# Kernel tuning notes

Hardware: AMD Instinct MI355X
Metric: run time of the kernel (lower is better)

Reference implementation:

```python
import jax, jax.numpy as jnp
import numpy as np

N, E = 100000, 1600000
F_IN, HID, C, L = 512, 128, 64, 64
ALPHA, THETA = 0.1, 0.5


def setup_inputs() -> dict:
    key = jax.random.key(0)
    ks = jax.random.split(key, 6)
    x = jax.random.normal(ks[0], (N, F_IN), jnp.float32)
    edge_index = jax.random.randint(ks[1], (2, E), 0, N, jnp.int32)
    W_in = jax.random.normal(ks[2], (F_IN, HID), jnp.float32) * (1.0 / np.sqrt(F_IN))
    b_in = jnp.zeros((HID,), jnp.float32)
    W_convs = jax.random.normal(ks[3], (L, HID, HID), jnp.float32) * (1.0 / np.sqrt(HID))
    W_out = jax.random.normal(ks[4], (HID, C), jnp.float32) * (1.0 / np.sqrt(HID))
    b_out = jnp.zeros((C,), jnp.float32)
    return {"x": x, "edge_index": edge_index, "W_in": W_in, "b_in": b_in,
            "W_convs": W_convs, "W_out": W_out, "b_out": b_out}


def reference(x, edge_index, W_in, b_in, W_convs, W_out, b_out):
    src, dst = edge_index[0], edge_index[1]
    # gcn_norm with self loops: A_hat = D^-1/2 (A + I) D^-1/2
    deg = jax.ops.segment_sum(jnp.ones((E,), x.dtype), dst, num_segments=N) + 1.0
    dinv = jax.lax.rsqrt(deg)
    ew = dinv[src] * dinv[dst]          # [E] off-diagonal weights
    self_w = dinv * dinv                # [N] self-loop weights

    def spmm(h):  # h: [N, HID]
        agg = jax.ops.segment_sum(h[src] * ew[:, None], dst, num_segments=N)
        return agg + self_w[:, None] * h

    # beta_l = log(theta / l + 1), l = 1..L
    betas = jnp.log(THETA / jnp.arange(1, L + 1, dtype=x.dtype) + 1.0)

    x0 = jax.nn.relu(x @ W_in + b_in)   # [N, HID]

    def layer(h, lw):
        W, beta = lw
        p = spmm(h)
        t = (1.0 - ALPHA) * p + ALPHA * x0          # initial residual
        out = (1.0 - beta) * t + beta * (t @ W)     # identity mapping (shared weights)
        return jax.nn.relu(out), None

    z, _ = jax.lax.scan(layer, x0, (W_convs, betas))
    logits = z @ W_out + b_out
    return z, jax.nn.log_softmax(logits, axis=-1)
```

## Files before the change

### kernel.cpp

```cpp
#include <hip/hip_runtime.h>
#include <hip/hip_bf16.h>

#define NN 100000
#define NE 1600000
#define F_IN 512
#define HID 128
#define C_OUT 64
#define L_LAYERS 64
#define SCAN_NB 98

using short8 = __attribute__((ext_vector_type(8))) short;
using f32x4  = __attribute__((ext_vector_type(4))) float;
typedef __attribute__((ext_vector_type(4))) unsigned short ushort4v;

__device__ __forceinline__ short f2bf(float f) {
    __hip_bfloat16 h = __float2bfloat16(f);
    return __builtin_bit_cast(short, h);
}
__device__ __forceinline__ unsigned short f2bfu(float f) {
    __hip_bfloat16 h = __float2bfloat16(f);
    return __builtin_bit_cast(unsigned short, h);
}
__device__ __forceinline__ float bflo(unsigned u) { return __uint_as_float(u << 16); }
__device__ __forceinline__ float bfhi(unsigned u) { return __uint_as_float(u & 0xffff0000u); }
__device__ __forceinline__ float bf2f(unsigned short u) { return __uint_as_float((unsigned)u << 16); }


__global__ void count_deg(const int* __restrict__ dst, int* __restrict__ cnt) {
    int e = blockIdx.x * blockDim.x + threadIdx.x;
    if (e < NE) atomicAdd(&cnt[dst[e]], 1);
}

__global__ void compute_dinv(const int* __restrict__ cnt, float* __restrict__ dinv) {
    int n = blockIdx.x * blockDim.x + threadIdx.x;
    if (n < NN) dinv[n] = rsqrtf((float)cnt[n] + 1.0f);
}

__global__ __launch_bounds__(256) void scan1(const int* __restrict__ cnt,
                                             int* __restrict__ row_ptr,
                                             int* __restrict__ partial) {
    __shared__ int sdata[256];
    int tid = threadIdx.x;
    int base = blockIdx.x * 1024;
    int v[4];
    int idx0 = base + tid * 4;
#pragma unroll
    for (int i = 0; i < 4; ++i) {
        int idx = idx0 + i;
        v[i] = (idx < NN) ? cnt[idx] : 0;
    }
    int s = v[0] + v[1] + v[2] + v[3];
    sdata[tid] = s;
    __syncthreads();
    int x = s;
    for (int off = 1; off < 256; off <<= 1) {
        int y = (tid >= off) ? sdata[tid - off] : 0;
        __syncthreads();
        x += y;
        sdata[tid] = x;
        __syncthreads();
    }
    int run = x - s;
#pragma unroll
    for (int i = 0; i < 4; ++i) {
        int idx = idx0 + i;
        if (idx < NN) row_ptr[idx] = run;
        run += v[i];
    }
    if (tid == 255) partial[blockIdx.x] = x;
}

__global__ __launch_bounds__(128) void scan2(int* __restrict__ partial) {
    __shared__ int sdata[128];
    int tid = threadIdx.x;
    int v = (tid < SCAN_NB) ? partial[tid] : 0;
    sdata[tid] = v;
    __syncthreads();
    int x = v;
    for (int off = 1; off < 128; off <<= 1) {
        int y = (tid >= off) ? sdata[tid - off] : 0;
        __syncthreads();
        x += y;
        sdata[tid] = x;
        __syncthreads();
    }
    if (tid < SCAN_NB) partial[tid] = x - v;
}

__global__ void scan3(int* __restrict__ row_ptr, const int* __restrict__ partial) {
    int idx = blockIdx.x * blockDim.x + threadIdx.x;
    if (idx < NN) row_ptr[idx] += partial[idx >> 10];
    else if (idx <= NN + 64) row_ptr[idx] = NE;
}

__global__ void scatter_csr(const int* __restrict__ src, const int* __restrict__ dst,
                            const float* __restrict__ dinv, int* __restrict__ fill,
                            int2* __restrict__ edges) {
    int e = blockIdx.x * blockDim.x + threadIdx.x;
    if (e >= NE) return;
    int s = src[e], d = dst[e];
    int pos = atomicAdd(&fill[d], 1);
    edges[pos] = make_int2(s, __float_as_int(dinv[s] * dinv[d]));
}

__global__ __launch_bounds__(256) void prep_wt(const float* __restrict__ Wc,
                                               const float* __restrict__ Win,
                                               __hip_bfloat16* __restrict__ WT,
                                               __hip_bfloat16* __restrict__ WinT) {
    int b = blockIdx.x, tid = threadIdx.x;
    if (b < 64) {
        const float* src = Wc + (size_t)b * HID * HID;
        __hip_bfloat16* dstp = WT + (size_t)b * HID * HID;
        for (int it = 0; it < 64; ++it) {
            int idx = it * 256 + tid;
            int n = idx >> 7, k = idx & 127;
            dstp[idx] = __float2bfloat16(src[k * HID + n]);
        }
    } else {
        int j = b - 64;
        for (int it = 0; it < 16; ++it) {
            int gid = j * 4096 + it * 256 + tid;
            int n = gid >> 9, k = gid & 511;
            WinT[gid] = __float2bfloat16(Win[k * HID + n]);
        }
    }
}

#define LOAD_SET(X0V, X1V, WVV, KT)                                              \
    {                                                                            \
        int k0_ = (KT) * 32;                                                     \
        _Pragma("unroll")                                                        \
        for (int i = 0; i < 2; ++i) {                                            \
            int id = i * 256 + tid;                                              \
            int rr = id >> 2, slot = id & 3;                                     \
            int grow = row0 + rr;                                                \
            X0V[i] = make_float4(0.f, 0.f, 0.f, 0.f); X1V[i] = X0V[i];           \
            if (grow < NN) {                                                     \
                X0V[i] = *(const float4*)&X[(size_t)grow * F_IN + k0_ + slot * 8];     \
                X1V[i] = *(const float4*)&X[(size_t)grow * F_IN + k0_ + slot * 8 + 4]; \
            }                                                                    \
            WVV[i] = *(const uint4*)&WinT[(size_t)rr * F_IN + k0_ + slot * 8];   \
        }                                                                        \
    }

#define PHASE(X0V, X1V, WVV, KT, BUF)                                            \
    {                                                                            \
        short* Xs = SMEM + (BUF) * 4096;                                         \
        short* Wsh = SMEM + 8192 + (BUF) * 4096;                                 \
        _Pragma("unroll")                                                        \
        for (int i = 0; i < 2; ++i) {                                            \
            int id = i * 256 + tid;                                              \
            int rr = id >> 2, slot = id & 3;                                     \
            short8 p;                                                            \
            p[0] = f2bf(X0V[i].x); p[1] = f2bf(X0V[i].y);                        \
            p[2] = f2bf(X0V[i].z); p[3] = f2bf(X0V[i].w);                        \
            p[4] = f2bf(X1V[i].x); p[5] = f2bf(X1V[i].y);                        \
            p[6] = f2bf(X1V[i].z); p[7] = f2bf(X1V[i].w);                        \
            *(short8*)&Xs[rr * 32 + (slot ^ ((rr >> 1) & 3)) * 8] = p;           \
            *(uint4*)&Wsh[rr * 32 + (slot ^ ((rr >> 1) & 3)) * 8] = WVV[i];      \
        }                                                                        \
        __syncthreads();                                                         \
        if ((KT) < 14) LOAD_SET(X0V, X1V, WVV, (KT) + 2);                        \
        short8 a[2], bb[8];                                                      \
        _Pragma("unroll")                                                        \
        for (int m = 0; m < 2; ++m) {                                            \
            int row = w * 32 + m * 16 + r;                                       \
            a[m] = *(short8*)&Xs[row * 32 + (g ^ ((row >> 1) & 3)) * 8];         \
        }                                                                        \
        _Pragma("unroll")                                                        \
        for (int n = 0; n < 8; ++n) {                                            \
            int row = n * 16 + r;                                                \
            bb[n] = *(short8*)&Wsh[row * 32 + (g ^ ((row >> 1) & 3)) * 8];       \
        }                                                                        \
        _Pragma("unroll")                                                        \
        for (int m = 0; m < 2; ++m)                                              \
            _Pragma("unroll")                                                    \
            for (int n = 0; n < 8; ++n)                                          \
                acc[m][n] = __builtin_amdgcn_mfma_f32_16x16x32_bf16(a[m], bb[n], acc[m][n], 0, 0, 0); \
    }

__global__ __launch_bounds__(256) void gemm_x0_mfma(const float* __restrict__ X,
                                                    const __hip_bfloat16* __restrict__ WinT,
                                                    const float* __restrict__ bias,
                                                    __hip_bfloat16* __restrict__ X0b) {
    __shared__ short SMEM[128 * 128];
    int tid = threadIdx.x;
    int w = tid >> 6, l = tid & 63, g = l >> 4, r = l & 15;
    int row0 = blockIdx.x * 128;
    f32x4 acc[2][8] = {};

    float4 ax0[2], ax1[2]; uint4 aw[2];
    float4 bx0[2], bx1[2]; uint4 bw[2];

    LOAD_SET(ax0, ax1, aw, 0);
    LOAD_SET(bx0, bx1, bw, 1);
    for (int kt = 0; kt < 16; kt += 2) {
        PHASE(ax0, ax1, aw, kt, 0);
        PHASE(bx0, bx1, bw, kt + 1, 1);
    }
    __syncthreads();
#pragma unroll
    for (int m = 0; m < 2; ++m) {
#pragma unroll
        for (int n = 0; n < 8; ++n) {
            int col = n * 16 + r;
            float bv = bias[col];
#pragma unroll
            for (int q = 0; q < 4; ++q) {
                int row = w * 32 + m * 16 + g * 4 + q;
                float v = fmaxf(acc[m][n][q] + bv, 0.f);
                SMEM[row * 128 + ((col >> 3) ^ (row & 15)) * 8 + (col & 7)] = f2bf(v);
            }
        }
    }
    __syncthreads();
#pragma unroll
    for (int i = 0; i < 8; ++i) {
        int id = i * 256 + tid;
        int rr = id >> 4, c8 = id & 15;
        int grow = row0 + rr;
        if (grow < NN)
            *(uint4*)&X0b[(size_t)grow * HID + c8 * 8] =
                *(uint4*)&SMEM[rr * 128 + ((c8 ^ (rr & 15)) * 8)];
    }
}

__global__ __launch_bounds__(512, 6) void layer_fused(const unsigned* __restrict__ H2,
                                                      const unsigned* __restrict__ X02,
                                                      const float* __restrict__ dinv,
                                                      const int* __restrict__ row_ptr,
                                                      const int2* __restrict__ edges,
                                                      const __hip_bfloat16* __restrict__ WTl,
                                                      float beta,
                                                      __hip_bfloat16* __restrict__ Hout,
                                                      float* __restrict__ Zf) {
    __shared__ short Ts[64 * 128];
    __shared__ short Ws[128 * 128];
    int tid = threadIdx.x;
    int w = tid >> 6, l = tid & 63, g = l >> 4, r = l & 15;
    int row0 = blockIdx.x * 64;

#pragma unroll
    for (int i = 0; i < 4; ++i) {
        int id = i * 512 + tid;
        int rr = id >> 4, slot = id & 15;
        uint4 wv = *(const uint4*)&WTl[(size_t)id * 8];
        *(uint4*)&Ws[rr * 128 + (slot ^ (rr & 15)) * 8] = wv;
    }

    unsigned* TsU = (unsigned*)Ts;
    int nb0 = row0 + w * 8;
    int ep[9];
#pragma unroll
    for (int k = 0; k < 9; ++k) ep[k] = __builtin_amdgcn_readfirstlane(row_ptr[nb0 + k]);

#pragma unroll
    for (int j = 0; j < 4; ++j) {
        int rrA = w * 8 + 2 * j, rrB = rrA + 1;
        int nA = row0 + rrA, nB = nA + 1;
        bool vA = nA < NN, vB = nB < NN;
        unsigned hsA = vA ? H2[((unsigned)nA << 6) + l] : 0u;
        unsigned hsB = vB ? H2[((unsigned)nB << 6) + l] : 0u;
        unsigned xvA = vA ? X02[((unsigned)nA << 6) + l] : 0u;
        unsigned xvB = vB ? X02[((unsigned)nB << 6) + l] : 0u;
        float dvA = vA ? dinv[nA] : 0.f, dvB = vB ? dinv[nB] : 0.f;
        float a0A = dvA * dvA * bflo(hsA), a1A = dvA * dvA * bfhi(hsA);
        float a0B = dvB * dvB * bflo(hsB), a1B = dvB * dvB * bfhi(hsB);
        int eA = ep[2 * j], e1A = ep[2 * j + 1];
        int eB = e1A, e1B = ep[2 * j + 2];
        while (eA < e1A || eB < e1B) {
            int cA = e1A - eA; cA = cA > 12 ? 12 : (cA < 0 ? 0 : cA);
            int cB = e1B - eB; cB = cB > 12 ? 12 : (cB < 0 ? 0 : cB);
            int sA[12], sB[12];
            float wA[12], wB[12];
#pragma unroll
            for (int u = 0; u < 12; ++u) {
                int2 t = edges[eA + u];
                sA[u] = (u < cA) ? t.x : 0;
                wA[u] = (u < cA) ? __int_as_float(t.y) : 0.f;
            }
#pragma unroll
            for (int u = 0; u < 12; ++u) {
                int2 t = edges[eB + u];
                sB[u] = (u < cB) ? t.x : 0;
                wB[u] = (u < cB) ? __int_as_float(t.y) : 0.f;
            }
            unsigned hvA[12], hvB[12];
#pragma unroll
            for (int u = 0; u < 12; ++u) hvA[u] = H2[((unsigned)sA[u] << 6) + l];
#pragma unroll
            for (int u = 0; u < 12; ++u) hvB[u] = H2[((unsigned)sB[u] << 6) + l];
#pragma unroll
            for (int u = 0; u < 12; ++u) {
                a0A = fmaf(wA[u], bflo(hvA[u]), a0A);
                a1A = fmaf(wA[u], bfhi(hvA[u]), a1A);
                a0B = fmaf(wB[u], bflo(hvB[u]), a0B);
                a1B = fmaf(wB[u], bfhi(hvB[u]), a1B);
            }
            eA += cA; eB += cB;
        }
        a0A = 0.9f * a0A + 0.1f * bflo(xvA);  a1A = 0.9f * a1A + 0.1f * bfhi(xvA);
        a0B = 0.9f * a0B + 0.1f * bflo(xvB);  a1B = 0.9f * a1B + 0.1f * bfhi(xvB);
        unsigned pkA = (unsigned)f2bfu(a0A) | ((unsigned)f2bfu(a1A) << 16);
        unsigned pkB = (unsigned)f2bfu(a0B) | ((unsigned)f2bfu(a1B) << 16);
        TsU[rrA * 64 + ((l >> 2) ^ (rrA & 15)) * 4 + (l & 3)] = pkA;
        TsU[rrB * 64 + ((l >> 2) ^ (rrB & 15)) * 4 + (l & 3)] = pkB;
    }
    __syncthreads();

    int nb = w & 3, cg = w >> 2;
    f32x4 acc[4] = {};
#pragma unroll
    for (int ks = 0; ks < 4; ++ks) {
        int rrT = nb * 16 + r;
        short8 bT = *(short8*)&Ts[rrT * 128 + ((ks * 4 + g) ^ (rrT & 15)) * 8];
        short8 aW[4];
#pragma unroll
        for (int c = 0; c < 4; ++c) {
            int rrW = (cg * 4 + c) * 16 + r;
            aW[c] = *(short8*)&Ws[rrW * 128 + ((ks * 4 + g) ^ (rrW & 15)) * 8];
        }
#pragma unroll
        for (int c = 0; c < 4; ++c)
            acc[c] = __builtin_amdgcn_mfma_f32_16x16x32_bf16(aW[c], bT, acc[c], 0, 0, 0);
    }

    float omb = 1.0f - beta;
    int node = nb * 16 + r;
    int grow = row0 + node;
    if (grow < NN) {
#pragma unroll
        for (int c = 0; c < 4; ++c) {
            int c0 = (cg * 4 + c) * 16 + g * 4;
            int slotE = c0 >> 3, posE = c0 & 7;
            ushort4v tv = *(ushort4v*)&Ts[node * 128 + (slotE ^ (node & 15)) * 8 + posE];
            float o[4];
#pragma unroll
            for (int q = 0; q < 4; ++q)
                o[q] = fmaxf(omb * bf2f(tv[q]) + beta * acc[c][q], 0.f);
            if (Zf) {
                *(float4*)&Zf[(size_t)grow * HID + c0] = make_float4(o[0], o[1], o[2], o[3]);
            } else {
                ushort4v hv;
#pragma unroll
                for (int q = 0; q < 4; ++q) hv[q] = f2bfu(o[q]);
                *(ushort4v*)&Hout[(size_t)grow * HID + c0] = hv;
            }
        }
    }
}

__global__ __launch_bounds__(256) void final_kernel(const float* __restrict__ Z,
                                                    const float* __restrict__ Wout,
                                                    const float* __restrict__ bout,
                                                    float* __restrict__ lo) {
    __shared__ float Wl[128 * 64];
    __shared__ float Zl[64][128];
    int tid = threadIdx.x;
    int w = tid >> 6, c = tid & 63;
    int n0 = blockIdx.x * 64;
#pragma unroll
    for (int i = 0; i < 8; ++i) {
        int id = i * 256 + tid;
        *(float4*)&Wl[id * 4] = *(const float4*)&Wout[(size_t)id * 4];
    }
#pragma unroll
    for (int i = 0; i < 8; ++i) {
        int id = i * 256 + tid;
        int rr = id >> 5, c4 = id & 31;
        int n = n0 + rr;
        float4 v = make_float4(0.f, 0.f, 0.f, 0.f);
        if (n < NN) v = *(const float4*)&Z[(size_t)n * HID + c4 * 4];
        *(float4*)&Zl[rr][c4 * 4] = v;
    }
    __syncthreads();
    float bv = bout[c];
#pragma unroll
    for (int i = 0; i < 4; ++i) {
        int nodeb = i * 16 + w * 4;
        float l0 = 0.f, l1 = 0.f, l2 = 0.f, l3 = 0.f;
#pragma unroll 8
        for (int k = 0; k < 128; ++k) {
            float wv = Wl[k * 64 + c];
            l0 = fmaf(Zl[nodeb + 0][k], wv, l0);
            l1 = fmaf(Zl[nodeb + 1][k], wv, l1);
            l2 = fmaf(Zl[nodeb + 2][k], wv, l2);
            l3 = fmaf(Zl[nodeb + 3][k], wv, l3);
        }
        float lg[4] = {l0 + bv, l1 + bv, l2 + bv, l3 + bv};
#pragma unroll
        for (int j = 0; j < 4; ++j) {
            float logit = lg[j];
            float m = logit;
#pragma unroll
            for (int off = 32; off; off >>= 1) m = fmaxf(m, __shfl_xor(m, off));
            float ex = __expf(logit - m);
            float ssum = ex;
#pragma unroll
            for (int off = 32; off; off >>= 1) ssum += __shfl_xor(ssum, off);
            int n = n0 + nodeb + j;
            if (n < NN) lo[(size_t)n * C_OUT + c] = logit - m - logf(ssum);
        }
    }
}

extern "C" void kernel_launch(void* const* d_in, const int* in_sizes, int n_in,
                              void* d_out, int out_size, void* d_ws, size_t ws_size,
                              hipStream_t stream) {
    const float* x = (const float*)d_in[0];
    const int* ei = (const int*)d_in[1];
    const int* src = ei;
    const int* dst = ei + NE;
    const float* W_in = (const float*)d_in[2];
    const float* b_in = (const float*)d_in[3];
    const float* W_convs = (const float*)d_in[4];
    const float* W_out = (const float*)d_in[5];
    const float* b_out = (const float*)d_in[6];
    float* out = (float*)d_out;

    char* ws = (char*)d_ws;
    float* dinv = (float*)ws;              ws += (size_t)NN * 4;
    int* row_ptr = (int*)ws;               ws += (size_t)(NN + 72) * 4;
    int* fill = (int*)ws;                  ws += (size_t)NN * 4;
    int* partial = (int*)ws;               ws += (size_t)128 * 4;
    int2* edges = (int2*)ws;               ws += (size_t)(NE + 32) * 8;
    __hip_bfloat16* WT = (__hip_bfloat16*)ws;   ws += (size_t)L_LAYERS * HID * HID * 2;
    __hip_bfloat16* WinT = (__hip_bfloat16*)ws; ws += (size_t)F_IN * HID * 2;
    __hip_bfloat16* x0b = (__hip_bfloat16*)ws;  ws += (size_t)NN * HID * 2;
    __hip_bfloat16* HbA = (__hip_bfloat16*)ws;  ws += (size_t)NN * HID * 2;
    __hip_bfloat16* HbB = (__hip_bfloat16*)ws;  ws += (size_t)NN * HID * 2;

    hipMemsetAsync(fill, 0, (size_t)NN * 4, stream);
    count_deg<<<(NE + 255) / 256, 256, 0, stream>>>(dst, fill);
    compute_dinv<<<(NN + 255) / 256, 256, 0, stream>>>(fill, dinv);
    scan1<<<SCAN_NB, 256, 0, stream>>>(fill, row_ptr, partial);
    scan2<<<1, 128, 0, stream>>>(partial);
    scan3<<<(NN + 255) / 256, 256, 0, stream>>>(row_ptr, partial);
    hipMemcpyAsync(fill, row_ptr, (size_t)NN * 4, hipMemcpyDeviceToDevice, stream);
    scatter_csr<<<(NE + 255) / 256, 256, 0, stream>>>(src, dst, dinv, fill, edges);
    prep_wt<<<80, 256, 0, stream>>>(W_convs, W_in, WT, WinT);

    int gemm_blocks = (NN + 127) / 128;
    gemm_x0_mfma<<<gemm_blocks, 256, 0, stream>>>(x, WinT, b_in, x0b);

    int layer_blocks = (NN + 63) / 64;
    float* zf = out;
    for (int l = 0; l < L_LAYERS; ++l) {
        const __hip_bfloat16* h_in = (l == 0) ? x0b : ((l & 1) ? HbA : HbB);
        __hip_bfloat16* h_out = (l & 1) ? HbB : HbA;
        float beta = logf(0.5f / (float)(l + 1) + 1.0f);
        bool last = (l == L_LAYERS - 1);
        layer_fused<<<layer_blocks, 512, 0, stream>>>(
            (const unsigned*)h_in, (const unsigned*)x0b, dinv, row_ptr, edges,
            WT + (size_t)l * HID * HID, beta,
            h_out, last ? zf : (float*)nullptr);
    }

    final_kernel<<<(NN + 63) / 64, 256, 0, stream>>>(zf, W_out, b_out, out + (size_t)NN * HID);
}
```

Before: 6.349 ms.

## Split wave across two nodes with 8-byte gathers and sort CSR neighbors

The SpMM gather now has each half-wave handle one of the two destination nodes. Each lane loads 8 bytes (4 bf16 features) per neighbor, and the per-iteration batch drops from 12 to 8 edges, which halves the number of gather instructions per edge. A new per-node bitonic sort orders each CSR row by source index to improve locality of the gathers, and a pad kernel zeroes the tail edges that unrolled loads read past the end. The added preprocessing costs one extra launch over all nodes, and the two half-waves can diverge when their node degrees differ.

```diff
diff --git a/kernel.cpp b/kernel.cpp
--- a/kernel.cpp
+++ b/kernel.cpp
@@ -101,6 +101,35 @@
     int s = src[e], d = dst[e];
     int pos = atomicAdd(&fill[d], 1);
     edges[pos] = make_int2(s, __float_as_int(dinv[s] * dinv[d]));
+}
+
+__global__ void pad_edges(int2* __restrict__ edges) {
+    int i = threadIdx.x;
+    if (i < 32) edges[NE + i] = make_int2(0, 0);
+}
+
+__global__ __launch_bounds__(64) void sort_edges(const int* __restrict__ row_ptr,
+                                                 int2* __restrict__ edges) {
+    int n = blockIdx.x;
+    int l = threadIdx.x;
+    int e0 = row_ptr[n], e1 = row_ptr[n + 1];
+    int deg = e1 - e0;
+    if (deg <= 1 || deg > 64) return;
+    int key = 0x7fffffff, val = 0;
+    if (l < deg) { int2 t = edges[e0 + l]; key = t.x; val = t.y; }
+#pragma unroll
+    for (int k = 2; k <= 64; k <<= 1) {
+#pragma unroll
+        for (int j = k >> 1; j > 0; j >>= 1) {
+            int pk = __shfl_xor(key, j);
+            int pv = __shfl_xor(val, j);
+            bool dir = ((l & k) == 0);
+            bool lowlane = ((l & j) == 0);
+            bool take = (pk < key) == (lowlane == dir);
+            if (take) { key = pk; val = pv; }
+        }
+    }
+    if (l < deg) edges[e0 + l] = make_int2(key, val);
 }
 
 __global__ __launch_bounds__(256) void prep_wt(const float* __restrict__ Wc,
@@ -225,8 +254,8 @@
     }
 }
 
-__global__ __launch_bounds__(512, 6) void layer_fused(const unsigned* __restrict__ H2,
-                                                      const unsigned* __restrict__ X02,
+__global__ __launch_bounds__(512, 6) void layer_fused(const uint2* __restrict__ H8,
+                                                      const uint2* __restrict__ X08,
                                                       const float* __restrict__ dinv,
                                                       const int* __restrict__ row_ptr,
                                                       const int2* __restrict__ edges,
@@ -238,6 +267,8 @@
     __shared__ short Ws[128 * 128];
     int tid = threadIdx.x;
     int w = tid >> 6, l = tid & 63, g = l >> 4, r = l & 15;
+    int h = l >> 5;
+    int q = l & 31;
     int row0 = blockIdx.x * 64;
 
 #pragma unroll
@@ -256,55 +287,50 @@
 
 #pragma unroll
     for (int j = 0; j < 4; ++j) {
-        int rrA = w * 8 + 2 * j, rrB = rrA + 1;
-        int nA = row0 + rrA, nB = nA + 1;
-        bool vA = nA < NN, vB = nB < NN;
-        unsigned hsA = vA ? H2[((unsigned)nA << 6) + l] : 0u;
-        unsigned hsB = vB ? H2[((unsigned)nB << 6) + l] : 0u;
-        unsigned xvA = vA ? X02[((unsigned)nA << 6) + l] : 0u;
-        unsigned xvB = vB ? X02[((unsigned)nB << 6) + l] : 0u;
-        float dvA = vA ? dinv[nA] : 0.f, dvB = vB ? dinv[nB] : 0.f;
-        float a0A = dvA * dvA * bflo(hsA), a1A = dvA * dvA * bfhi(hsA);
-        float a0B = dvB * dvB * bflo(hsB), a1B = dvB * dvB * bfhi(hsB);
+        int rrA = w * 8 + 2 * j;
+        int nA = row0 + rrA;
+        int myn = nA + h;
+        bool vmy = myn < NN;
+        uint2 hs = vmy ? H8[(size_t)(unsigned)myn * 32 + q] : make_uint2(0u, 0u);
+        uint2 xv = vmy ? X08[(size_t)(unsigned)myn * 32 + q] : make_uint2(0u, 0u);
+        float dv = vmy ? dinv[myn] : 0.f;
+        float sw = dv * dv;
+        float a0 = sw * bflo(hs.x), a1 = sw * bfhi(hs.x);
+        float a2 = sw * bflo(hs.y), a3 = sw * bfhi(hs.y);
         int eA = ep[2 * j], e1A = ep[2 * j + 1];
         int eB = e1A, e1B = ep[2 * j + 2];
         while (eA < e1A || eB < e1B) {
-            int cA = e1A - eA; cA = cA > 12 ? 12 : (cA < 0 ? 0 : cA);
-            int cB = e1B - eB; cB = cB > 12 ? 12 : (cB < 0 ? 0 : cB);
-            int sA[12], sB[12];
-            float wA[12], wB[12];
-#pragma unroll
-            for (int u = 0; u < 12; ++u) {
-                int2 t = edges[eA + u];
-                sA[u] = (u < cA) ? t.x : 0;
-                wA[u] = (u < cA) ? __int_as_float(t.y) : 0.f;
+            int cA = e1A - eA; cA = cA > 8 ? 8 : (cA < 0 ? 0 : cA);
+            int cB = e1B - eB; cB = cB > 8 ? 8 : (cB < 0 ? 0 : cB);
+            int ebase = h ? eB : eA;
+            int cmy  = h ? cB : cA;
+            int2 em[8];
+#pragma unroll
+            for (int u = 0; u < 8; ++u) em[u] = edges[ebase + u];
+            uint2 hv[8];
+            float ww[8];
+#pragma unroll
+            for (int u = 0; u < 8; ++u) {
+                int s = (u < cmy) ? em[u].x : 0;
+                ww[u] = (u < cmy) ? __int_as_float(em[u].y) : 0.f;
+                hv[u] = H8[(size_t)(unsigned)s * 32 + q];
             }
 #pragma unroll
-            for (int u = 0; u < 12; ++u) {
-                int2 t = edges[eB + u];
-                sB[u] = (u < cB) ? t.x : 0;
-                wB[u] = (u < cB) ? __int_as_float(t.y) : 0.f;
-            }
-            unsigned hvA[12], hvB[12];
-#pragma unroll
-            for (int u = 0; u < 12; ++u) hvA[u] = H2[((unsigned)sA[u] << 6) + l];
-#pragma unroll
-            for (int u = 0; u < 12; ++u) hvB[u] = H2[((unsigned)sB[u] << 6) + l];
-#pragma unroll
-            for (int u = 0; u < 12; ++u) {
-                a0A = fmaf(wA[u], bflo(hvA[u]), a0A);
-                a1A = fmaf(wA[u], bfhi(hvA[u]), a1A);
-                a0B = fmaf(wB[u], bflo(hvB[u]), a0B);
-                a1B = fmaf(wB[u], bfhi(hvB[u]), a1B);
+            for (int u = 0; u < 8; ++u) {
+                a0 = fmaf(ww[u], bflo(hv[u].x), a0);
+                a1 = fmaf(ww[u], bfhi(hv[u].x), a1);
+                a2 = fmaf(ww[u], bflo(hv[u].y), a2);
+                a3 = fmaf(ww[u], bfhi(hv[u].y), a3);
             }
             eA += cA; eB += cB;
         }
-        a0A = 0.9f * a0A + 0.1f * bflo(xvA);  a1A = 0.9f * a1A + 0.1f * bfhi(xvA);
-        a0B = 0.9f * a0B + 0.1f * bflo(xvB);  a1B = 0.9f * a1B + 0.1f * bfhi(xvB);
-        unsigned pkA = (unsigned)f2bfu(a0A) | ((unsigned)f2bfu(a1A) << 16);
-        unsigned pkB = (unsigned)f2bfu(a0B) | ((unsigned)f2bfu(a1B) << 16);
-        TsU[rrA * 64 + ((l >> 2) ^ (rrA & 15)) * 4 + (l & 3)] = pkA;
-        TsU[rrB * 64 + ((l >> 2) ^ (rrB & 15)) * 4 + (l & 3)] = pkB;
+        a0 = 0.9f * a0 + 0.1f * bflo(xv.x);  a1 = 0.9f * a1 + 0.1f * bfhi(xv.x);
+        a2 = 0.9f * a2 + 0.1f * bflo(xv.y);  a3 = 0.9f * a3 + 0.1f * bfhi(xv.y);
+        unsigned pk0 = (unsigned)f2bfu(a0) | ((unsigned)f2bfu(a1) << 16);
+        unsigned pk1 = (unsigned)f2bfu(a2) | ((unsigned)f2bfu(a3) << 16);
+        int rr = rrA + h;
+        *(uint2*)&TsU[rr * 64 + (((q >> 1) ^ (rr & 15)) << 2) + (q & 1) * 2] =
+            make_uint2(pk0, pk1);
     }
     __syncthreads();
 
@@ -336,15 +362,15 @@
             ushort4v tv = *(ushort4v*)&Ts[node * 128 + (slotE ^ (node & 15)) * 8 + posE];
             float o[4];
 #pragma unroll
-            for (int q = 0; q < 4; ++q)
-                o[q] = fmaxf(omb * bf2f(tv[q]) + beta * acc[c][q], 0.f);
+            for (int p = 0; p < 4; ++p)
+                o[p] = fmaxf(omb * bf2f(tv[p]) + beta * acc[c][p], 0.f);
             if (Zf) {
                 *(float4*)&Zf[(size_t)grow * HID + c0] = make_float4(o[0], o[1], o[2], o[3]);
             } else {
-                ushort4v hv;
-#pragma unroll
-                for (int q = 0; q < 4; ++q) hv[q] = f2bfu(o[q]);
-                *(ushort4v*)&Hout[(size_t)grow * HID + c0] = hv;
+                ushort4v hvv;
+#pragma unroll
+                for (int p = 0; p < 4; ++p) hvv[p] = f2bfu(o[p]);
+                *(ushort4v*)&Hout[(size_t)grow * HID + c0] = hvv;
             }
         }
     }
@@ -438,6 +464,8 @@
     scan3<<<(NN + 255) / 256, 256, 0, stream>>>(row_ptr, partial);
     hipMemcpyAsync(fill, row_ptr, (size_t)NN * 4, hipMemcpyDeviceToDevice, stream);
     scatter_csr<<<(NE + 255) / 256, 256, 0, stream>>>(src, dst, dinv, fill, edges);
+    pad_edges<<<1, 32, 0, stream>>>(edges);
+    sort_edges<<<NN, 64, 0, stream>>>(row_ptr, edges);
     prep_wt<<<80, 256, 0, stream>>>(W_convs, W_in, WT, WinT);
 
     int gemm_blocks = (NN + 127) / 128;
@@ -451,7 +479,7 @@
         float beta = logf(0.5f / (float)(l + 1) + 1.0f);
         bool last = (l == L_LAYERS - 1);
         layer_fused<<<layer_blocks, 512, 0, stream>>>(
-            (const unsigned*)h_in, (const unsigned*)x0b, dinv, row_ptr, edges,
+            (const uint2*)h_in, (const uint2*)x0b, dinv, row_ptr, edges,
             WT + (size_t)l * HID * HID, beta,
             h_out, last ? zf : (float*)nullptr);
     }
```

Result: slower. 6.546 ms (+3.1%).
